# Kernel tuning notes

Measured on AMD Instinct MI355X. Metric: run time of the kernel, lower is better.

The kernel has to match this reference:

```python
import jax, jax.numpy as jnp
import numpy as np

_SAMPLING_EPS = 1e-5


def setup_inputs() -> dict:
    key = jax.random.key(0)
    k1, k2, k3, k4, k5, k6 = jax.random.split(key, 6)
    B, V = 128, 128000
    return {
        "logits": jax.random.normal(k1, (B, V), dtype=jnp.float32),
        "temperature": jax.random.uniform(k2, (B,), dtype=jnp.float32),
        "min_p": jax.random.uniform(k3, (B,), dtype=jnp.float32),
        "top_k": jax.random.randint(k4, (B,), 0, 1024),
        "top_p": jax.random.uniform(k5, (B,), dtype=jnp.float32),
        "q": jax.random.uniform(k6, (B, V), dtype=jnp.float32),
        "num_logprobs": 20,
    }


def reference(logits, temperature, min_p, top_k, top_p, q, num_logprobs):
    B, V = logits.shape
    # raw logprobs computed BEFORE any processing (as in Sampler.forward)
    raw_logprobs = jax.nn.log_softmax(logits, axis=-1)
    # greedy sample on unscaled logits
    greedy = jnp.argmax(logits, axis=-1)
    # temperature scaling
    lt = logits / temperature[:, None]
    # min-p filtering
    probs = jax.nn.softmax(lt, axis=-1)
    max_p = jnp.max(probs, axis=-1, keepdims=True)
    lt = jnp.where(probs >= min_p[:, None] * max_p, lt, -jnp.inf)
    # top-k / top-p filtering on ascending-sorted logits (vLLM style)
    idx = jnp.argsort(lt, axis=-1)                       # ascending
    ls = jnp.take_along_axis(lt, idx, axis=-1)
    k = jnp.clip(top_k, 1, V)
    kth = jnp.take_along_axis(ls, (V - k)[:, None], axis=-1)  # k-th largest value
    ls = jnp.where(ls < kth, -jnp.inf, ls)
    ps = jax.nn.softmax(ls, axis=-1)
    csum = jnp.cumsum(ps, axis=-1)
    pmask = csum <= (1.0 - top_p)[:, None]
    pmask = pmask.at[:, -1].set(False)                   # always keep the max token
    ls = jnp.where(pmask, -jnp.inf, ls)
    inv = jnp.argsort(idx, axis=-1)                      # inverse permutation (scatter back)
    filtered = jnp.take_along_axis(ls, inv, axis=-1)
    # exponential-race sampling: argmax(probs / Exp(1)) ~ Categorical(probs)
    probs2 = jax.nn.softmax(filtered, axis=-1)
    expo = -jnp.log(jnp.clip(q, 1e-10, 1.0))
    rand_sampled = jnp.argmax(probs2 / expo, axis=-1)
    sampled = jnp.where(temperature < _SAMPLING_EPS, greedy, rand_sampled)
    # gather_logprobs: top-k logprobs + sampled-token logprob + rank
    topk_lp, topk_idx = jax.lax.top_k(raw_logprobs, num_logprobs)
    tok_lp = jnp.take_along_axis(raw_logprobs, sampled[:, None], axis=-1)  # (B,1)
    ranks = jnp.sum(raw_logprobs >= tok_lp, axis=-1)
    out_idx = jnp.concatenate([sampled[:, None], topk_idx], axis=1).astype(jnp.int32)
    out_lp = jnp.concatenate([tok_lp, topk_lp], axis=1)  # (B, num_logprobs+1)
    return (sampled[:, None].astype(jnp.int32), out_idx, out_lp, ranks)
```

## Files before the change

### kernel.cpp

```cpp
#include <hip/hip_runtime.h>
#include <math.h>

#define NB 1024
#define C_CAP 2048
#define BLK 1024
#define PRECAP 4096
#define FLOORB 682
#define BIN_SCALE ((float)NB / 12.0f)

__device__ __forceinline__ int bin_of(float x) {
  int b = (int)floorf((x + 6.0f) * BIN_SCALE);
  return min(max(b, 0), NB - 1);
}
__device__ __forceinline__ unsigned long long pack_vi(float v, int idx) {
  return ((unsigned long long)__float_as_uint(v) << 32) | (unsigned int)idx;
}
__device__ __forceinline__ unsigned long long okey(float v, int idx) {
  unsigned int u = __float_as_uint(v);
  u = (u & 0x80000000u) ? ~u : (u | 0x80000000u);
  return ((unsigned long long)u << 32) | (unsigned long long)(0x7fffffffu - (unsigned int)idx);
}
__device__ __forceinline__ float okey_val(unsigned long long k) {
  unsigned int hi = (unsigned int)(k >> 32);
  unsigned int u = (hi & 0x80000000u) ? (hi & 0x7fffffffu) : ~hi;
  return __uint_as_float(u);
}
__device__ __forceinline__ int okey_idx(unsigned long long k) {
  return (int)(0x7fffffffu - (unsigned int)k);
}

__global__ __launch_bounds__(BLK)
void sampler_fused(const float* __restrict__ logits,
                   const float* __restrict__ temperature,
                   const float* __restrict__ min_p,
                   const int* __restrict__ top_k,
                   const float* __restrict__ top_p,
                   const float* __restrict__ q,
                   const int* __restrict__ nl_ptr,
                   int V, int B,
                   float* __restrict__ out) {
  const int row = blockIdx.x, tid = threadIdx.x;
  __shared__ int h[NB + 1];
  __shared__ int cur[NB];
  __shared__ unsigned long long lst[PRECAP];
  __shared__ unsigned long long bkt[C_CAP];
  __shared__ float sv[C_CAP];
  __shared__ int   si[C_CAP];
  __shared__ float ss[C_CAP];
  __shared__ float st[BLK];
  __shared__ float rf[BLK], rf2[BLK];
  __shared__ int   ri[BLK];
  __shared__ int   s_fail, s_b, s_cnt;
  __shared__ float s_lse;

  for (int i = tid; i < NB; i += BLK) { h[i] = 0; cur[i] = 0; }
  if (tid == 0) { s_b = 0; s_cnt = 0; h[NB] = 0; }
  __syncthreads();

  const float* lrow = logits + (size_t)row * V;
  float sum = 0.0f;
  const int n4 = V >> 2;
  const float4* p4 = (const float4*)lrow;
  int i = tid;
  for (; i + BLK < n4; i += 2 * BLK) {
    float4 a = p4[i], b2 = p4[i + BLK];
    float va[8] = {a.x, a.y, a.z, a.w, b2.x, b2.y, b2.z, b2.w};
    int ia[8];
    #pragma unroll
    for (int c2 = 0; c2 < 4; c2++) { ia[c2] = (i << 2) + c2; ia[c2 + 4] = ((i + BLK) << 2) + c2; }
    #pragma unroll
    for (int c2 = 0; c2 < 8; c2++) {
      float x = va[c2];
      int b = bin_of(x);
      atomicAdd(&h[b], 1);
      sum += __expf(fminf(x, 70.0f) - 6.0f);
      if (b >= FLOORB) {
        int p = atomicAdd(&s_cnt, 1);
        if (p < PRECAP) lst[p] = pack_vi(x, ia[c2]);
      }
    }
  }
  for (; i < n4; i += BLK) {
    float4 a = p4[i];
    float va[4] = {a.x, a.y, a.z, a.w};
    #pragma unroll
    for (int c2 = 0; c2 < 4; c2++) {
      float x = va[c2];
      int b = bin_of(x);
      atomicAdd(&h[b], 1);
      sum += __expf(fminf(x, 70.0f) - 6.0f);
      if (b >= FLOORB) {
        int p = atomicAdd(&s_cnt, 1);
        if (p < PRECAP) lst[p] = pack_vi(x, (i << 2) + c2);
      }
    }
  }
  for (int j = (n4 << 2) + tid; j < V; j += BLK) {
    float x = lrow[j];
    int b = bin_of(x);
    atomicAdd(&h[b], 1);
    sum += __expf(fminf(x, 70.0f) - 6.0f);
    if (b >= FLOORB) {
      int p = atomicAdd(&s_cnt, 1);
      if (p < PRECAP) lst[p] = pack_vi(x, j);
    }
  }
  __syncthreads();

  st[tid] = sum;
  __syncthreads();
  for (int s = BLK / 2; s > 0; s >>= 1) {
    if (tid < s) st[tid] += st[tid + s];
    __syncthreads();
  }
  if (tid == 0) s_lse = 6.0f + logf(st[0]);

  for (int off = 1; off < NB; off <<= 1) {
    int t0 = (tid + off < NB) ? h[tid + off] : 0;
    __syncthreads();
    h[tid] += t0;
    __syncthreads();
  }
  int nl = nl_ptr[0];
  int ke = top_k[row]; ke = min(max(ke, 1), V);
  int Kp = max(ke, nl);
  if (h[tid] >= Kp) atomicMax(&s_b, tid);
  __syncthreads();
  const int bstar = s_b;
  const int total_pre = s_cnt;
  const bool fast = (bstar >= FLOORB) && (total_pre <= PRECAP);
  int c = min(h[bstar], C_CAP); if (c < 1) c = 1;

  if (fast) {
    int m = min(total_pre, PRECAP);
    for (int j = tid; j < m; j += BLK) {
      unsigned long long kk = lst[j];
      float x = __uint_as_float((unsigned int)(kk >> 32));
      int idx = (int)(unsigned int)kk;
      int b = bin_of(x);
      if (b >= bstar) {
        int a = atomicAdd(&cur[b], 1);
        int pos = h[b + 1] + a;
        if (pos < C_CAP) bkt[pos] = okey(x, idx);
      }
    }
  } else {
    for (int ii = tid; ii < n4; ii += BLK) {
      float4 a4 = p4[ii];
      float va[4] = {a4.x, a4.y, a4.z, a4.w};
      #pragma unroll
      for (int c2 = 0; c2 < 4; c2++) {
        int b = bin_of(va[c2]);
        if (b >= bstar) {
          int a = atomicAdd(&cur[b], 1);
          int pos = h[b + 1] + a;
          if (pos < C_CAP) bkt[pos] = okey(va[c2], (ii << 2) + c2);
        }
      }
    }
    for (int j = (n4 << 2) + tid; j < V; j += BLK) {
      float x = lrow[j];
      int b = bin_of(x);
      if (b >= bstar) {
        int a = atomicAdd(&cur[b], 1);
        int pos = h[b + 1] + a;
        if (pos < C_CAP) bkt[pos] = okey(x, j);
      }
    }
  }
  __syncthreads();

  for (int pos = tid; pos < c; pos += BLK) {
    unsigned long long k0 = bkt[pos];
    float v = okey_val(k0);
    int b = bin_of(v);
    int gs = h[b + 1];
    int ge = min(h[b], c);
    int rk = 0;
    for (int j = gs; j < ge; j++) if (bkt[j] > k0) rk++;
    int fin = gs + rk;
    sv[fin] = v; si[fin] = okey_idx(k0);
  }
  __syncthreads();

  float temp = temperature[row];
  bool ug = (temp < 1e-5f);
  float rt = 1.0f / (ug ? 1.0f : temp);
  float mp = min_p[row], tp = top_p[row];
  ke = min(ke, c);
  float v0 = sv[0];
  float lt0 = v0 * rt;

  float ltk = sv[ke - 1] * rt;
  float kth = (expf(ltk - lt0) >= mp) ? ltk : -INFINITY;

  if (tid == 0) s_fail = c;
  __syncthreads();
  for (int ii = tid; ii < c; ii += BLK) {
    float ltj = sv[ii] * rt;
    if (!((expf(ltj - lt0) >= mp) && (ltj >= kth))) { atomicMin(&s_fail, ii); break; }
  }
  __syncthreads();
  int n1 = s_fail; if (n1 < 1) n1 = 1;
  __syncthreads();

  int L = (c + BLK - 1) / BLK;
  int base = tid * L;
  int lim = min(base + L, c);
  float run = 0.0f;
  for (int j = base; j < lim; j++) {
    float pj = (j < n1) ? expf(sv[j] * rt - lt0) : 0.0f;
    run += pj; ss[j] = run;
  }
  st[tid] = run;
  __syncthreads();
  for (int off = 1; off < BLK; off <<= 1) {
    float t0 = (tid >= off) ? st[tid - off] : 0.0f;
    __syncthreads();
    st[tid] += t0;
    __syncthreads();
  }
  float offv = (tid > 0) ? st[tid - 1] : 0.0f;
  for (int j = base; j < lim; j++) ss[j] += offv;
  __syncthreads();
  float Z1 = ss[n1 - 1];

  if (tid == 0) s_fail = n1;
  __syncthreads();
  for (int ii = tid; ii < n1; ii += BLK) {
    if (ii > 0 && !((1.0f - ss[ii - 1] / Z1) > (1.0f - tp))) { atomicMin(&s_fail, ii); break; }
  }
  __syncthreads();
  int n2 = s_fail; if (n2 < 1) n2 = 1;
  __syncthreads();
  float Z2 = ss[n2 - 1];

  const float* qrow = q + (size_t)row * V;
  float bsc = -INFINITY; int bidx = 0x7fffffff; float bval = 0.0f;
  for (int ii = tid; ii < n2; ii += BLK) {
    float pj = expf(sv[ii] * rt - lt0);
    float qv = qrow[si[ii]];
    qv = fminf(fmaxf(qv, 1e-10f), 1.0f);
    float sc = (pj / Z2) / (-logf(qv));
    if (sc > bsc || (sc == bsc && si[ii] < bidx)) { bsc = sc; bidx = si[ii]; bval = sv[ii]; }
  }
  rf[tid] = bsc; ri[tid] = bidx; rf2[tid] = bval;
  __syncthreads();
  for (int s = BLK / 2; s > 0; s >>= 1) {
    if (tid < s) {
      if (rf[tid + s] > rf[tid] ||
          (rf[tid + s] == rf[tid] && ri[tid + s] < ri[tid])) {
        rf[tid] = rf[tid + s]; ri[tid] = ri[tid + s]; rf2[tid] = rf2[tid + s];
      }
    }
    __syncthreads();
  }
  int sampled = ug ? si[0] : ri[0];
  float val_s = ug ? sv[0] : rf2[0];
  float lse = s_lse;
  float tok_lp = val_s - lse;
  __syncthreads();

  if (tid == 0) s_fail = c;
  __syncthreads();
  for (int ii = tid; ii < c; ii += BLK)
    if (!((sv[ii] - lse) >= tok_lp)) { atomicMin(&s_fail, ii); break; }
  __syncthreads();
  int rank = s_fail;

  int W = nl + 1;
  if (tid == 0) {
    out[row] = (float)sampled;
    out[B + row * W] = (float)sampled;
    out[B + B * W + row * W] = tok_lp;
    out[B + 2 * B * W + row] = (float)rank;
  }
  for (int t = tid; t < nl; t += BLK) {
    out[B + row * W + 1 + t] = (float)si[t];
    out[B + B * W + row * W + 1 + t] = sv[t] - lse;
  }
}

extern "C" void kernel_launch(void* const* d_in, const int* in_sizes, int n_in,
                              void* d_out, int out_size, void* d_ws, size_t ws_size,
                              hipStream_t stream) {
  const float* logits      = (const float*)d_in[0];
  const float* temperature = (const float*)d_in[1];
  const float* min_p       = (const float*)d_in[2];
  const int*   top_k       = (const int*)d_in[3];
  const float* top_p       = (const float*)d_in[4];
  const float* q           = (const float*)d_in[5];
  const int*   nl_ptr      = (const int*)d_in[6];

  int B = in_sizes[1];
  int V = in_sizes[0] / B;
  float* out = (float*)d_out;

  hipLaunchKernelGGL(sampler_fused, dim3(B), dim3(BLK), 0, stream,
                     logits, temperature, min_p, top_k, top_p, q, nl_ptr,
                     V, B, out);
}
```

Measured before the change: 167.2 us.

## Split row scan into two-block prefilter kernel with wave-aggregated candidate append

Splits the single fused per-row kernel into two launches. The first scans each half-row in its own 512-thread block (256 blocks total), computing partial exp-sums and appending candidates above a fixed value bound with wave-level ballot aggregation instead of per-element shared atomics and a full histogram. The second kernel builds the histogram only from the gathered candidates, then does the existing selection and sampling work, falling back to a full-row rescan if the candidates are too many or too few. This aims to use more of the device's compute units and to drop the per-element histogram atomics, at the cost of an extra launch and a round trip through global workspace.

Result: slower. 174.5 us (+4.4%).

```diff
diff --git a/kernel.cpp b/kernel.cpp
--- a/kernel.cpp
+++ b/kernel.cpp
@@ -3,10 +3,12 @@
 
 #define NB 1024
 #define C_CAP 2048
-#define BLK 1024
-#define PRECAP 4096
+#define BLK1 512
+#define BLK2 1024
+#define LCAP2 2048
 #define FLOORB 682
 #define BIN_SCALE ((float)NB / 12.0f)
+#define BOUND 1.9921875f
 
 __device__ __forceinline__ int bin_of(float x) {
   int b = (int)floorf((x + 6.0f) * BIN_SCALE);
@@ -29,91 +31,165 @@
   return (int)(0x7fffffffu - (unsigned int)k);
 }
 
-__global__ __launch_bounds__(BLK)
-void sampler_fused(const float* __restrict__ logits,
-                   const float* __restrict__ temperature,
-                   const float* __restrict__ min_p,
-                   const int* __restrict__ top_k,
-                   const float* __restrict__ top_p,
-                   const float* __restrict__ q,
-                   const int* __restrict__ nl_ptr,
-                   int V, int B,
-                   float* __restrict__ out) {
-  const int row = blockIdx.x, tid = threadIdx.x;
-  __shared__ int h[NB + 1];
-  __shared__ int cur[NB];
-  __shared__ unsigned long long lst[PRECAP];
-  __shared__ unsigned long long bkt[C_CAP];
-  __shared__ float sv[C_CAP];
-  __shared__ int   si[C_CAP];
-  __shared__ float ss[C_CAP];
-  __shared__ float st[BLK];
-  __shared__ float rf[BLK], rf2[BLK];
-  __shared__ int   ri[BLK];
-  __shared__ int   s_fail, s_b, s_cnt;
-  __shared__ float s_lse;
-
-  for (int i = tid; i < NB; i += BLK) { h[i] = 0; cur[i] = 0; }
-  if (tid == 0) { s_b = 0; s_cnt = 0; h[NB] = 0; }
-  __syncthreads();
-
+__global__ __launch_bounds__(BLK1)
+void k1_scan(const float* __restrict__ logits, int V, int halfElems,
+             unsigned long long* __restrict__ plist, int* __restrict__ pcnt,
+             float* __restrict__ psum) {
+  const int row = blockIdx.y, half = blockIdx.x, tid = threadIdx.x;
+  const int lane = tid & 63;
   const float* lrow = logits + (size_t)row * V;
+  const int start = half * halfElems;
+  const int end = min(start + halfElems, V);
+  __shared__ unsigned long long lst[LCAP2];
+  __shared__ float rs[BLK1];
+  __shared__ int lcnt;
+  if (tid == 0) lcnt = 0;
+  __syncthreads();
   float sum = 0.0f;
-  const int n4 = V >> 2;
-  const float4* p4 = (const float4*)lrow;
+  const int n = max(end - start, 0);
+  const int n4 = n >> 2;
+  const float4* p4 = (const float4*)(lrow + start);
   int i = tid;
-  for (; i + BLK < n4; i += 2 * BLK) {
-    float4 a = p4[i], b2 = p4[i + BLK];
+  for (; i + BLK1 < n4; i += 2 * BLK1) {
+    float4 a = p4[i], b2 = p4[i + BLK1];
     float va[8] = {a.x, a.y, a.z, a.w, b2.x, b2.y, b2.z, b2.w};
     int ia[8];
     #pragma unroll
-    for (int c2 = 0; c2 < 4; c2++) { ia[c2] = (i << 2) + c2; ia[c2 + 4] = ((i + BLK) << 2) + c2; }
+    for (int c2 = 0; c2 < 4; c2++) { ia[c2] = (i << 2) + c2; ia[c2 + 4] = ((i + BLK1) << 2) + c2; }
     #pragma unroll
     for (int c2 = 0; c2 < 8; c2++) {
       float x = va[c2];
-      int b = bin_of(x);
-      atomicAdd(&h[b], 1);
       sum += __expf(fminf(x, 70.0f) - 6.0f);
-      if (b >= FLOORB) {
-        int p = atomicAdd(&s_cnt, 1);
-        if (p < PRECAP) lst[p] = pack_vi(x, ia[c2]);
-      }
-    }
-  }
-  for (; i < n4; i += BLK) {
+      bool pred = (x >= BOUND);
+      unsigned long long mk = __ballot(pred);
+      if (mk) {
+        int leader = __ffsll((long long)mk) - 1;
+        int base = 0;
+        if (lane == leader) base = atomicAdd(&lcnt, __popcll(mk));
+        base = __shfl(base, leader, 64);
+        if (pred) {
+          int p = base + __popcll(mk & ((1ull << lane) - 1ull));
+          if (p < LCAP2) lst[p] = pack_vi(x, start + ia[c2]);
+        }
+      }
+    }
+  }
+  for (; i < n4; i += BLK1) {
     float4 a = p4[i];
     float va[4] = {a.x, a.y, a.z, a.w};
     #pragma unroll
     for (int c2 = 0; c2 < 4; c2++) {
       float x = va[c2];
-      int b = bin_of(x);
-      atomicAdd(&h[b], 1);
       sum += __expf(fminf(x, 70.0f) - 6.0f);
-      if (b >= FLOORB) {
-        int p = atomicAdd(&s_cnt, 1);
-        if (p < PRECAP) lst[p] = pack_vi(x, (i << 2) + c2);
-      }
-    }
-  }
-  for (int j = (n4 << 2) + tid; j < V; j += BLK) {
-    float x = lrow[j];
-    int b = bin_of(x);
-    atomicAdd(&h[b], 1);
+      bool pred = (x >= BOUND);
+      unsigned long long mk = __ballot(pred);
+      if (mk) {
+        int leader = __ffsll((long long)mk) - 1;
+        int base = 0;
+        if (lane == leader) base = atomicAdd(&lcnt, __popcll(mk));
+        base = __shfl(base, leader, 64);
+        if (pred) {
+          int p = base + __popcll(mk & ((1ull << lane) - 1ull));
+          if (p < LCAP2) lst[p] = pack_vi(x, start + (i << 2) + c2);
+        }
+      }
+    }
+  }
+  for (int j = (n4 << 2) + tid; j < n; j += BLK1) {
+    float x = lrow[start + j];
     sum += __expf(fminf(x, 70.0f) - 6.0f);
-    if (b >= FLOORB) {
-      int p = atomicAdd(&s_cnt, 1);
-      if (p < PRECAP) lst[p] = pack_vi(x, j);
-    }
-  }
-  __syncthreads();
-
-  st[tid] = sum;
-  __syncthreads();
-  for (int s = BLK / 2; s > 0; s >>= 1) {
-    if (tid < s) st[tid] += st[tid + s];
-    __syncthreads();
-  }
-  if (tid == 0) s_lse = 6.0f + logf(st[0]);
+    bool pred = (x >= BOUND);
+    unsigned long long mk = __ballot(pred);
+    if (mk) {
+      int leader = __ffsll((long long)mk) - 1;
+      int base = 0;
+      if (lane == leader) base = atomicAdd(&lcnt, __popcll(mk));
+      base = __shfl(base, leader, 64);
+      if (pred) {
+        int p = base + __popcll(mk & ((1ull << lane) - 1ull));
+        if (p < LCAP2) lst[p] = pack_vi(x, start + j);
+      }
+    }
+  }
+  __syncthreads();
+  rs[tid] = sum;
+  __syncthreads();
+  for (int s = BLK1 / 2; s > 0; s >>= 1) {
+    if (tid < s) rs[tid] += rs[tid + s];
+    __syncthreads();
+  }
+  const size_t rc = (size_t)row * 2 + half;
+  if (tid == 0) { psum[rc] = rs[0]; pcnt[rc] = lcnt; }
+  int m = min(lcnt, LCAP2);
+  unsigned long long* prow = plist + rc * LCAP2;
+  for (int j = tid; j < m; j += BLK1) prow[j] = lst[j];
+}
+
+__global__ __launch_bounds__(BLK2)
+void k2_fused(const float* __restrict__ logits,
+              const float* __restrict__ temperature,
+              const float* __restrict__ min_p,
+              const int* __restrict__ top_k,
+              const float* __restrict__ top_p,
+              const float* __restrict__ q,
+              const int* __restrict__ nl_ptr,
+              int V, int B,
+              const unsigned long long* __restrict__ plist,
+              const int* __restrict__ pcnt,
+              const float* __restrict__ psum,
+              float* __restrict__ out) {
+  const int row = blockIdx.x, tid = threadIdx.x;
+  __shared__ int h[NB + 1];
+  __shared__ int cur[NB];
+  __shared__ unsigned long long lst[2 * LCAP2];
+  __shared__ unsigned long long bkt[C_CAP];
+  __shared__ float sv[C_CAP];
+  __shared__ int   si[C_CAP];
+  __shared__ float ss[C_CAP];
+  __shared__ float st[BLK2];
+  __shared__ float rf[BLK2], rf2[BLK2];
+  __shared__ int   ri[BLK2];
+  __shared__ int   s_fail, s_b;
+  __shared__ float s_lse;
+
+  for (int i = tid; i < NB; i += BLK2) { h[i] = 0; cur[i] = 0; }
+  if (tid == 0) { s_b = 0; h[NB] = 0; }
+  __syncthreads();
+
+  const int p0 = pcnt[(size_t)row * 2], p1 = pcnt[(size_t)row * 2 + 1];
+  const int c0 = min(p0, LCAP2), c1 = min(p1, LCAP2);
+  const int tot = c0 + c1;
+  int nl = nl_ptr[0];
+  int ke = top_k[row]; ke = min(max(ke, 1), V);
+  const int Kp = max(ke, nl);
+  const bool fast = (p0 <= LCAP2) && (p1 <= LCAP2) && (tot >= Kp);
+
+  if (tid == 0) s_lse = 6.0f + logf(psum[(size_t)row * 2] + psum[(size_t)row * 2 + 1]);
+
+  const float* lrow = logits + (size_t)row * V;
+  const int n4 = V >> 2;
+  const float4* p4 = (const float4*)lrow;
+
+  if (fast) {
+    const unsigned long long* pr0 = plist + (size_t)row * 2 * LCAP2;
+    const unsigned long long* pr1 = pr0 + LCAP2;
+    for (int j = tid; j < c0; j += BLK2) lst[j] = pr0[j];
+    for (int j = tid; j < c1; j += BLK2) lst[c0 + j] = pr1[j];
+    __syncthreads();
+    for (int j = tid; j < tot; j += BLK2) {
+      float x = __uint_as_float((unsigned int)(lst[j] >> 32));
+      atomicAdd(&h[bin_of(x)], 1);
+    }
+  } else {
+    for (int ii = tid; ii < n4; ii += BLK2) {
+      float4 a4 = p4[ii];
+      atomicAdd(&h[bin_of(a4.x)], 1); atomicAdd(&h[bin_of(a4.y)], 1);
+      atomicAdd(&h[bin_of(a4.z)], 1); atomicAdd(&h[bin_of(a4.w)], 1);
+    }
+    for (int j = (n4 << 2) + tid; j < V; j += BLK2)
+      atomicAdd(&h[bin_of(lrow[j])], 1);
+  }
+  __syncthreads();
 
   for (int off = 1; off < NB; off <<= 1) {
     int t0 = (tid + off < NB) ? h[tid + off] : 0;
@@ -121,19 +197,13 @@
     h[tid] += t0;
     __syncthreads();
   }
-  int nl = nl_ptr[0];
-  int ke = top_k[row]; ke = min(max(ke, 1), V);
-  int Kp = max(ke, nl);
   if (h[tid] >= Kp) atomicMax(&s_b, tid);
   __syncthreads();
   const int bstar = s_b;
-  const int total_pre = s_cnt;
-  const bool fast = (bstar >= FLOORB) && (total_pre <= PRECAP);
   int c = min(h[bstar], C_CAP); if (c < 1) c = 1;
 
   if (fast) {
-    int m = min(total_pre, PRECAP);
-    for (int j = tid; j < m; j += BLK) {
+    for (int j = tid; j < tot; j += BLK2) {
       unsigned long long kk = lst[j];
       float x = __uint_as_float((unsigned int)(kk >> 32));
       int idx = (int)(unsigned int)kk;
@@ -145,7 +215,7 @@
       }
     }
   } else {
-    for (int ii = tid; ii < n4; ii += BLK) {
+    for (int ii = tid; ii < n4; ii += BLK2) {
       float4 a4 = p4[ii];
       float va[4] = {a4.x, a4.y, a4.z, a4.w};
       #pragma unroll
@@ -158,7 +228,7 @@
         }
       }
     }
-    for (int j = (n4 << 2) + tid; j < V; j += BLK) {
+    for (int j = (n4 << 2) + tid; j < V; j += BLK2) {
       float x = lrow[j];
       int b = bin_of(x);
       if (b >= bstar) {
@@ -170,7 +240,7 @@
   }
   __syncthreads();
 
-  for (int pos = tid; pos < c; pos += BLK) {
+  for (int pos = tid; pos < c; pos += BLK2) {
     unsigned long long k0 = bkt[pos];
     float v = okey_val(k0);
     int b = bin_of(v);
@@ -196,7 +266,7 @@
 
   if (tid == 0) s_fail = c;
   __syncthreads();
-  for (int ii = tid; ii < c; ii += BLK) {
+  for (int ii = tid; ii < c; ii += BLK2) {
     float ltj = sv[ii] * rt;
     if (!((expf(ltj - lt0) >= mp) && (ltj >= kth))) { atomicMin(&s_fail, ii); break; }
   }
@@ -204,7 +274,7 @@
   int n1 = s_fail; if (n1 < 1) n1 = 1;
   __syncthreads();
 
-  int L = (c + BLK - 1) / BLK;
+  int L = (c + BLK2 - 1) / BLK2;
   int base = tid * L;
   int lim = min(base + L, c);
   float run = 0.0f;
@@ -214,7 +284,7 @@
   }
   st[tid] = run;
   __syncthreads();
-  for (int off = 1; off < BLK; off <<= 1) {
+  for (int off = 1; off < BLK2; off <<= 1) {
     float t0 = (tid >= off) ? st[tid - off] : 0.0f;
     __syncthreads();
     st[tid] += t0;
@@ -227,7 +297,7 @@
 
   if (tid == 0) s_fail = n1;
   __syncthreads();
-  for (int ii = tid; ii < n1; ii += BLK) {
+  for (int ii = tid; ii < n1; ii += BLK2) {
     if (ii > 0 && !((1.0f - ss[ii - 1] / Z1) > (1.0f - tp))) { atomicMin(&s_fail, ii); break; }
   }
   __syncthreads();
@@ -237,7 +307,7 @@
 
   const float* qrow = q + (size_t)row * V;
   float bsc = -INFINITY; int bidx = 0x7fffffff; float bval = 0.0f;
-  for (int ii = tid; ii < n2; ii += BLK) {
+  for (int ii = tid; ii < n2; ii += BLK2) {
     float pj = expf(sv[ii] * rt - lt0);
     float qv = qrow[si[ii]];
     qv = fminf(fmaxf(qv, 1e-10f), 1.0f);
@@ -246,7 +316,7 @@
   }
   rf[tid] = bsc; ri[tid] = bidx; rf2[tid] = bval;
   __syncthreads();
-  for (int s = BLK / 2; s > 0; s >>= 1) {
+  for (int s = BLK2 / 2; s > 0; s >>= 1) {
     if (tid < s) {
       if (rf[tid + s] > rf[tid] ||
           (rf[tid + s] == rf[tid] && ri[tid + s] < ri[tid])) {
@@ -263,7 +333,7 @@
 
   if (tid == 0) s_fail = c;
   __syncthreads();
-  for (int ii = tid; ii < c; ii += BLK)
+  for (int ii = tid; ii < c; ii += BLK2)
     if (!((sv[ii] - lse) >= tok_lp)) { atomicMin(&s_fail, ii); break; }
   __syncthreads();
   int rank = s_fail;
@@ -275,7 +345,7 @@
     out[B + B * W + row * W] = tok_lp;
     out[B + 2 * B * W + row] = (float)rank;
   }
-  for (int t = tid; t < nl; t += BLK) {
+  for (int t = tid; t < nl; t += BLK2) {
     out[B + row * W + 1 + t] = (float)si[t];
     out[B + B * W + row * W + 1 + t] = sv[t] - lse;
   }
@@ -295,8 +365,16 @@
   int B = in_sizes[1];
   int V = in_sizes[0] / B;
   float* out = (float*)d_out;
-
-  hipLaunchKernelGGL(sampler_fused, dim3(B), dim3(BLK), 0, stream,
+  int halfElems = (((V + 1) / 2) + 3) & ~3;
+
+  unsigned char* w = (unsigned char*)d_ws;
+  unsigned long long* plist = (unsigned long long*)w; w += (size_t)B * 2 * LCAP2 * sizeof(unsigned long long);
+  int* pcnt = (int*)w;                                w += (size_t)B * 2 * sizeof(int);
+  float* psum = (float*)w;                            w += (size_t)B * 2 * sizeof(float);
+
+  hipLaunchKernelGGL(k1_scan, dim3(2, B), dim3(BLK1), 0, stream,
+                     logits, V, halfElems, plist, pcnt, psum);
+  hipLaunchKernelGGL(k2_fused, dim3(B), dim3(BLK2), 0, stream,
                      logits, temperature, min_p, top_k, top_p, q, nl_ptr,
-                     V, B, out);
-}
+                     V, B, plist, pcnt, psum, out);
+}
```
